# Optimization experiments

Hardware: AMD Instinct MI355X
Metric: run time of the kernel (lower is better)

Reference implementation:

```python
import jax, jax.numpy as jnp
import numpy as np
import math

EMBD_SIZE = 1024
OUT_SIZE = 1024
B, N = 8, 2048

def setup_inputs() -> dict:
    key = jax.random.key(0)
    k1, k2, k3 = jax.random.split(key, 3)
    embd = jax.random.normal(k1, (B, N, EMBD_SIZE), dtype=jnp.float32)
    # nn.Linear(embd_size, out_size): weight [out, in], bias [out]
    bound = 1.0 / math.sqrt(EMBD_SIZE)
    W = jax.random.uniform(k2, (OUT_SIZE, EMBD_SIZE), dtype=jnp.float32, minval=-bound, maxval=bound)
    b = jax.random.uniform(k3, (OUT_SIZE,), dtype=jnp.float32, minval=-bound, maxval=bound)
    return {"embd": embd, "W": W, "b": b}

def reference(embd, W, b):
    # c = Linear(embd): [B, N, out_size]
    c = jnp.einsum('bne,oe->bno', embd, W) + b
    # scores = c @ c^T / sqrt(embd_size), softmax over last dim
    score = jnp.einsum('bno,bmo->bnm', c, c) / jnp.sqrt(jnp.float32(EMBD_SIZE))
    score = jax.nn.softmax(score, axis=-1)
    # output = score @ c : [B, N, out_size]
    return jnp.einsum('bnm,bmo->bno', score, c)
```

## Files before the change

kernel.cpp:

```cpp
#include <hip/hip_runtime.h>

typedef unsigned short u16;
typedef unsigned int u32;
typedef __attribute__((ext_vector_type(8))) short short8;
typedef __attribute__((ext_vector_type(4))) float f32x4;

__device__ inline u16 f2bf(float f) {
  u32 x = __float_as_uint(f);
  x += 0x7fff + ((x >> 16) & 1);
  return (u16)(x >> 16);
}
__device__ inline float bf2f(u16 h) {
  return __uint_as_float(((u32)h) << 16);
}
__device__ inline void gload16(const void* g, void* l) {
  __builtin_amdgcn_global_load_lds((const __attribute__((address_space(1))) u32*)g,
                                   (__attribute__((address_space(3))) u32*)l, 16, 0, 0);
}

__device__ inline int stile_off(int rg, int cg) {
  return rg * 128 + ((((cg >> 3) ^ ((rg >> 3) & 7)) << 3)) + (cg & 7);
}

__global__ void cast_all(const float* __restrict__ embd, const float* __restrict__ W,
                         u16* __restrict__ embd_b, u16* __restrict__ W_b) {
  const float* src; u16* dst; size_t i;
  if (blockIdx.x < 16384) {
    src = embd; dst = embd_b;
    i = ((size_t)blockIdx.x * 256 + threadIdx.x) * 4;
  } else {
    src = W; dst = W_b;
    i = ((size_t)(blockIdx.x - 16384) * 256 + threadIdx.x) * 4;
  }
  float4 v = *(const float4*)(src + i);
  ushort4 o;
  o.x = f2bf(v.x); o.y = f2bf(v.y); o.z = f2bf(v.z); o.w = f2bf(v.w);
  *(ushort4*)(dst + i) = o;
}

#define BM 128
#define BN 128
#define BK 32

template<int MODE>
__global__ __launch_bounds__(256, 2)
void gemm_nt(const u16* __restrict__ A, const u16* __restrict__ B,
             float* __restrict__ Cf, u16* __restrict__ Cb, u16* __restrict__ CT,
             const float* __restrict__ bias, float* __restrict__ rowsum,
             int M, int N, int K, float scale, long sA, long sB, long sC)
{
  __shared__ __align__(16) char smem[32768];
  u16* As = (u16*)smem;
  u16* Bs = As + BM * BK;
  u16* stile = (u16*)smem;
  float* stf = (float*)smem;

  int z, mBase, nBase, bi = 0, bj = 0;
  if (MODE == 0) {
    z = 0;
    mBase = blockIdx.y * BM;
    nBase = blockIdx.x * BN;
  } else if (MODE == 1) {
    z = blockIdx.x;
    int t = blockIdx.y, row = 0;
    const int nb = N >> 7;
    while (t >= nb - row) { t -= nb - row; ++row; }
    bi = row; bj = row + t;
    mBase = bi * BM; nBase = bj * BN;
  } else {
    z = blockIdx.x;
    nBase = (blockIdx.y & 7) * BN;
    mBase = (blockIdx.y >> 3) * BM;
  }

  A += (size_t)z * sA;
  B += (size_t)z * sB;
  if (MODE == 2) Cf += (size_t)z * sC; else Cb += (size_t)z * sC;
  if (MODE != 0) rowsum += (size_t)z * M;

  const int tid  = threadIdx.x;
  const int lane = tid & 63;
  const int wave = tid >> 6;
  const int wm = (wave >> 1) * 64;
  const int wn = (wave & 1) * 64;
  const int q = lane >> 4;
  const int r = lane & 15;

  const int lo0 = tid * 16;
  const int lo1 = lo0 + 4096;
  const int row0 = lo0 >> 6, kc0 = (lo0 & 63) >> 1;
  const int row1 = lo1 >> 6, kc1 = (lo1 & 63) >> 1;

  const u16* a0 = A + (size_t)(mBase + row0) * K + kc0;
  const u16* a1 = A + (size_t)(mBase + row1) * K + kc1;
  const u16* b0 = B + (size_t)(nBase + row0) * K + kc0;
  const u16* b1 = B + (size_t)(nBase + row1) * K + kc1;

  f32x4 acc[4][4] = {};

  for (int k0 = 0; k0 < K; k0 += BK) {
    gload16(a0 + k0, (char*)As + lo0);
    gload16(a1 + k0, (char*)As + lo1);
    gload16(b0 + k0, (char*)Bs + lo0);
    gload16(b1 + k0, (char*)Bs + lo1);
    __syncthreads();

    short8 af[4], bfr[4];
#pragma unroll
    for (int t = 0; t < 4; ++t) {
      af[t]  = *(const short8*)(As + (wm + t * 16 + r) * BK + q * 8);
      bfr[t] = *(const short8*)(Bs + (wn + t * 16 + r) * BK + q * 8);
    }
#pragma unroll
    for (int mi = 0; mi < 4; ++mi)
#pragma unroll
      for (int ni = 0; ni < 4; ++ni)
        acc[mi][ni] = __builtin_amdgcn_mfma_f32_16x16x32_bf16(af[mi], bfr[ni], acc[mi][ni], 0, 0, 0);
    __syncthreads();
  }


  if (MODE == 0) {
    float bv[4];
#pragma unroll
    for (int ni = 0; ni < 4; ++ni) bv[ni] = bias[nBase + wn + ni * 16 + r];
#pragma unroll
    for (int mi = 0; mi < 4; ++mi)
#pragma unroll
      for (int ni = 0; ni < 4; ++ni)
#pragma unroll
        for (int reg = 0; reg < 4; ++reg) {
          int rl = wm + mi * 16 + q * 4 + reg;
          int cl = wn + ni * 16 + r;
          stile[stile_off(rl, cl)] = f2bf(acc[mi][ni][reg] + bv[ni]);
        }
    __syncthreads();
    {
      const int z1 = mBase >> 11;
      const int n0 = mBase & 2047;
      u16* ctb = CT + (size_t)z1 * 1024 * 2048;
#pragma unroll
      for (int rnd = 0; rnd < 8; ++rnd) {
        int idx = rnd * 256 + tid;
        int ch = idx & 15, n = idx >> 4;
        short8 v = *(const short8*)(stile + n * 128 + ((ch ^ ((n >> 3) & 7)) << 3));
        *(short8*)(Cb + (size_t)(mBase + n) * N + nBase + ch * 8) = v;
      }
#pragma unroll
      for (int rnd = 0; rnd < 8; ++rnd) {
        int idx = rnd * 256 + tid;
        int ch = idx & 15, cc = idx >> 4;
        short8 v;
#pragma unroll
        for (int j = 0; j < 8; ++j) v[j] = (short)stile[stile_off(ch * 8 + j, cc)];
        *(short8*)(ctb + (size_t)(nBase + cc) * 2048 + n0 + ch * 8) = v;
      }
    }
  } else if (MODE == 1) {
    const bool mirror = (bi != bj);
    float colacc[4] = {0.f, 0.f, 0.f, 0.f};
#pragma unroll
    for (int mi = 0; mi < 4; ++mi) {
      float rs[4] = {0.f, 0.f, 0.f, 0.f};
#pragma unroll
      for (int ni = 0; ni < 4; ++ni)
#pragma unroll
        for (int reg = 0; reg < 4; ++reg) {
          float e = __expf(acc[mi][ni][reg] * scale);
          u16 h = f2bf(e);
          float f = bf2f(h);
          rs[reg] += f;
          if (mirror) colacc[ni] += f;
          stile[stile_off(wm + mi * 16 + q * 4 + reg, wn + ni * 16 + r)] = h;
        }
#pragma unroll
      for (int reg = 0; reg < 4; ++reg) {
        float v = rs[reg];
        v += __shfl_xor(v, 1);
        v += __shfl_xor(v, 2);
        v += __shfl_xor(v, 4);
        v += __shfl_xor(v, 8);
        if (r == 0)
          atomicAdd(&rowsum[mBase + wm + mi * 16 + q * 4 + reg], v);
      }
    }
    if (mirror) {
#pragma unroll
      for (int ni = 0; ni < 4; ++ni) {
        float v = colacc[ni];
        v += __shfl_xor(v, 16);
        v += __shfl_xor(v, 32);
        if (q == 0)
          atomicAdd(&rowsum[nBase + wn + ni * 16 + r], v);
      }
    }
    __syncthreads();
#pragma unroll
    for (int rnd = 0; rnd < 8; ++rnd) {
      int idx = rnd * 256 + tid;
      int ch = idx & 15, n = idx >> 4;
      short8 v = *(const short8*)(stile + n * 128 + ((ch ^ ((n >> 3) & 7)) << 3));
      *(short8*)(Cb + (size_t)(mBase + n) * N + nBase + ch * 8) = v;
    }
    if (mirror) {
#pragma unroll
      for (int rnd = 0; rnd < 8; ++rnd) {
        int idx = rnd * 256 + tid;
        int ch = idx & 15, cc = idx >> 4;
        short8 v;
#pragma unroll
        for (int j = 0; j < 8; ++j) v[j] = (short)stile[stile_off(ch * 8 + j, cc)];
        *(short8*)(Cb + (size_t)(nBase + cc) * N + mBase + ch * 8) = v;
      }
    }
  } else {
#pragma unroll
    for (int p = 0; p < 2; ++p) {
      if ((wave >> 1) == p) {
#pragma unroll
        for (int mi = 0; mi < 4; ++mi)
#pragma unroll
          for (int reg = 0; reg < 4; ++reg) {
            int lr = mi * 16 + q * 4 + reg;
            float inv = 1.0f / rowsum[mBase + wm + lr];
#pragma unroll
            for (int ni = 0; ni < 4; ++ni)
              stf[lr * 128 + wn + ni * 16 + r] = acc[mi][ni][reg] * inv;
          }
      }
      __syncthreads();
#pragma unroll
      for (int rnd = 0; rnd < 8; ++rnd) {
        int idx = rnd * 256 + tid;
        int n = idx >> 5, ch = idx & 31;
        float4 v = *(const float4*)(stf + n * 128 + ch * 4);
        *(float4*)(Cf + (size_t)(mBase + p * 64 + n) * N + nBase + ch * 4) = v;
      }
      __syncthreads();
    }
  }
}

extern "C" void kernel_launch(void* const* d_in, const int* in_sizes, int n_in,
                              void* d_out, int out_size, void* d_ws, size_t ws_size,
                              hipStream_t stream) {
  const float* embd = (const float*)d_in[0];
  const float* W    = (const float*)d_in[1];
  const float* bias = (const float*)d_in[2];
  float* out = (float*)d_out;

  char* ws = (char*)d_ws;
  u16* P_b    = (u16*)(ws + 0);
  u16* embd_b = (u16*)(ws + 0);
  u16* W_b    = (u16*)(ws + 33554432);
  u16* c_b    = (u16*)(ws + 67108864);
  u16* cT_b   = (u16*)(ws + 100663296);
  float* rowsum = (float*)(ws + 134217728);

  cast_all<<<17408, 256, 0, stream>>>(embd, W, embd_b, W_b);

  gemm_nt<0><<<dim3(8, 128, 1), 256, 0, stream>>>(
      embd_b, W_b, nullptr, c_b, cT_b, bias, nullptr,
      16384, 1024, 1024, 0.f, 0, 0, 0);

  hipMemsetAsync(rowsum, 0, 16384 * sizeof(float), stream);

  gemm_nt<1><<<dim3(8, 136, 1), 256, 0, stream>>>(
      c_b, c_b, nullptr, P_b, nullptr, nullptr, rowsum,
      2048, 2048, 1024, 0.03125f, 2048L * 1024, 2048L * 1024, 2048L * 2048);

  gemm_nt<2><<<dim3(8, 128, 1), 256, 0, stream>>>(
      P_b, cT_b, out, nullptr, nullptr, nullptr, rowsum,
      2048, 1024, 2048, 0.f, 2048L * 2048, 2048L * 1024, 2048L * 1024);
}
```

Measured before the change: 321.3 us.

## Double K tile to 64 with XOR-swizzled LDS layout for GEMM operands

After: 294.8 us. 8.3% less time.

```diff
diff --git a/kernel.cpp b/kernel.cpp
--- a/kernel.cpp
+++ b/kernel.cpp
@@ -18,8 +18,11 @@
                                    (__attribute__((address_space(3))) u32*)l, 16, 0, 0);
 }
 
-__device__ inline int stile_off(int rg, int cg) {
-  return rg * 128 + ((((cg >> 3) ^ ((rg >> 3) & 7)) << 3)) + (cg & 7);
+__device__ inline int sg(int r) {
+  return ((r >> 3) & 7) ^ (((r >> 2) & 1) << 2) ^ (((r >> 3) & 1) << 1);
+}
+__device__ inline int stile_off(int rl, int cl) {
+  return rl * 128 + (((cl >> 3) ^ sg(rl)) << 3) + (cl & 7);
 }
 
 __global__ void cast_all(const float* __restrict__ embd, const float* __restrict__ W,
@@ -40,7 +43,7 @@
 
 #define BM 128
 #define BN 128
-#define BK 32
+#define BK 64
 
 template<int MODE>
 __global__ __launch_bounds__(256, 2)
@@ -85,37 +88,41 @@
   const int wn = (wave & 1) * 64;
   const int q = lane >> 4;
   const int r = lane & 15;
-
-  const int lo0 = tid * 16;
-  const int lo1 = lo0 + 4096;
-  const int row0 = lo0 >> 6, kc0 = (lo0 & 63) >> 1;
-  const int row1 = lo1 >> 6, kc1 = (lo1 & 63) >> 1;
-
-  const u16* a0 = A + (size_t)(mBase + row0) * K + kc0;
-  const u16* a1 = A + (size_t)(mBase + row1) * K + kc1;
-  const u16* b0 = B + (size_t)(nBase + row0) * K + kc0;
-  const u16* b1 = B + (size_t)(nBase + row1) * K + kc1;
+  const int rswz = r & 7;
+
+  const int srow = tid >> 3;
+  const int scol = ((tid & 7) ^ (srow & 7)) * 8;
+  const int lds0 = tid * 16;
+
+  const u16* a0 = A + (size_t)(mBase + srow) * K + scol;
+  const u16* b0 = B + (size_t)(nBase + srow) * K + scol;
 
   f32x4 acc[4][4] = {};
 
   for (int k0 = 0; k0 < K; k0 += BK) {
-    gload16(a0 + k0, (char*)As + lo0);
-    gload16(a1 + k0, (char*)As + lo1);
-    gload16(b0 + k0, (char*)Bs + lo0);
-    gload16(b1 + k0, (char*)Bs + lo1);
-    __syncthreads();
-
-    short8 af[4], bfr[4];
-#pragma unroll
-    for (int t = 0; t < 4; ++t) {
-      af[t]  = *(const short8*)(As + (wm + t * 16 + r) * BK + q * 8);
-      bfr[t] = *(const short8*)(Bs + (wn + t * 16 + r) * BK + q * 8);
-    }
-#pragma unroll
-    for (int mi = 0; mi < 4; ++mi)
-#pragma unroll
-      for (int ni = 0; ni < 4; ++ni)
-        acc[mi][ni] = __builtin_amdgcn_mfma_f32_16x16x32_bf16(af[mi], bfr[ni], acc[mi][ni], 0, 0, 0);
+#pragma unroll
+    for (int i = 0; i < 4; ++i)
+      gload16(a0 + (size_t)(32 * i) * K + k0, (char*)As + lds0 + i * 4096);
+#pragma unroll
+    for (int i = 0; i < 4; ++i)
+      gload16(b0 + (size_t)(32 * i) * K + k0, (char*)Bs + lds0 + i * 4096);
+    __syncthreads();
+
+#pragma unroll
+    for (int kk = 0; kk < 2; ++kk) {
+      short8 af[4], bfr[4];
+#pragma unroll
+      for (int t = 0; t < 4; ++t) {
+        const int go = (((kk * 4 + q) ^ rswz)) * 8;
+        af[t]  = *(const short8*)(As + (wm + t * 16 + r) * BK + go);
+        bfr[t] = *(const short8*)(Bs + (wn + t * 16 + r) * BK + go);
+      }
+#pragma unroll
+      for (int mi = 0; mi < 4; ++mi)
+#pragma unroll
+        for (int ni = 0; ni < 4; ++ni)
+          acc[mi][ni] = __builtin_amdgcn_mfma_f32_16x16x32_bf16(af[mi], bfr[ni], acc[mi][ni], 0, 0, 0);
+    }
     __syncthreads();
   }
 
@@ -143,7 +150,7 @@
       for (int rnd = 0; rnd < 8; ++rnd) {
         int idx = rnd * 256 + tid;
         int ch = idx & 15, n = idx >> 4;
-        short8 v = *(const short8*)(stile + n * 128 + ((ch ^ ((n >> 3) & 7)) << 3));
+        short8 v = *(const short8*)(stile + n * 128 + ((ch ^ sg(n)) << 3));
         *(short8*)(Cb + (size_t)(mBase + n) * N + nBase + ch * 8) = v;
       }
 #pragma unroll
@@ -199,7 +206,7 @@
     for (int rnd = 0; rnd < 8; ++rnd) {
       int idx = rnd * 256 + tid;
       int ch = idx & 15, n = idx >> 4;
-      short8 v = *(const short8*)(stile + n * 128 + ((ch ^ ((n >> 3) & 7)) << 3));
+      short8 v = *(const short8*)(stile + n * 128 + ((ch ^ sg(n)) << 3));
       *(short8*)(Cb + (size_t)(mBase + n) * N + nBase + ch * 8) = v;
     }
     if (mirror) {
```
